# Performance work log

Hardware: AMD Instinct MI355X
Metric: run time of the kernel (lower is better)

## Reference

```python
import jax, jax.numpy as jnp
import numpy as np

DIM = 512
H = 8
HD = DIM // H
SCALE = HD ** (-0.5)


def setup_inputs() -> dict:
    key = jax.random.key(0)
    ks = jax.random.split(key, 10)
    B, Lq, Lp, V = 8, 64, 512, 32
    query = jax.random.normal(ks[0], (B, Lq, DIM), dtype=jnp.float32)
    memory = jax.random.normal(ks[1], (B, Lp, V, DIM), dtype=jnp.float32)
    init = lambda k: jax.random.normal(k, (DIM, DIM), dtype=jnp.float32) * (DIM ** -0.5)
    return {
        "query": query,
        "memory": memory,
        "Wq_c": init(ks[2]),
        "Wk_c": init(ks[3]),
        "Wv_c": init(ks[4]),
        "Wq": init(ks[5]),
        "Wk": init(ks[6]),
        "Wv": init(ks[7]),
        "Wp": init(ks[8]),
        "bp": jnp.zeros((DIM,), dtype=jnp.float32),
    }


def reference(query, memory, Wq_c, Wk_c, Wv_c, Wq, Wk, Wv, Wp, bp):
    B, Lq, d = query.shape
    _, Lp, V, _ = memory.shape
    # ---- stage 1: channel cross-attention over V ----
    qc = (query @ Wq_c).reshape(B, H, Lq, HD)                 # raw view split (faithful)
    kc = (memory @ Wk_c).mean(axis=1).reshape(B, H, V, HD)    # mean over L_p, then view
    vc = (memory @ Wv_c).reshape(B, H, Lp, V, HD)             # 5D value tensor
    # NOTE: original divides by scale = head_dim**-0.5 (i.e. multiplies by sqrt(hd))
    ch_scores = jnp.einsum('bhqd,bhvd->bhqv', qc, kc) / SCALE
    ch_weights = jax.nn.softmax(ch_scores, axis=-1)
    # einsum contracts BOTH q and v (faithful to 'bnqv,bnlvd->bnld')
    ch_out = jnp.einsum('bhqv,bhlvd->bhld', ch_weights, vc)   # (B,H,Lp,HD)
    mem_agg = ch_out.transpose(0, 2, 1, 3).reshape(B, Lp, d)
    # ---- stage 2: standard MHA, query attends to aggregated memory ----
    Q = (query @ Wq).reshape(B, Lq, H, HD).transpose(0, 2, 1, 3)
    K = (mem_agg @ Wk).reshape(B, Lp, H, HD).transpose(0, 2, 1, 3)
    Vv = (mem_agg @ Wv).reshape(B, Lp, H, HD).transpose(0, 2, 1, 3)
    scores = jnp.einsum('bhqd,bhkd->bhqk', Q, K) / SCALE
    weights = jax.nn.softmax(scores, axis=-1)
    attn = jnp.einsum('bhqk,bhkd->bhqd', weights, Vv)
    out = attn.transpose(0, 2, 1, 3).reshape(B, Lq, d)
    return out @ Wp + bp
```

## Files before the change

kernel.cpp:

```cpp
#include <hip/hip_runtime.h>
#include <math.h>

#define NB 8
#define LQ 64
#define LP 512
#define NV 32
#define DIM 512
#define NH 8
#define HD 64

typedef __attribute__((ext_vector_type(4))) float f32x4;
typedef __attribute__((ext_vector_type(8))) short s16x8;

__device__ __forceinline__ unsigned short f2bf(float x) {
  unsigned int u = __float_as_uint(x);
  u += 0x7fff + ((u >> 16) & 1);
  return (unsigned short)(u >> 16);
}
__device__ __forceinline__ float bf2f(unsigned short h) {
  return __uint_as_float(((unsigned int)h) << 16);
}

__global__ __launch_bounds__(256) void k_part(const float* __restrict__ mem,
                                              float* __restrict__ part) {
  int blk = blockIdx.x;
  int bv = blk >> 3, ch = blk & 7;
  int b = bv >> 5, v = bv & 31;
  int tid = threadIdx.x;
  float a0 = 0.f, a1 = 0.f;
  int l0 = ch * 64;
  for (int l = l0; l < l0 + 64; ++l) {
    const float* row = mem + (((size_t)b * LP + l) * NV + v) * DIM;
    a0 += row[tid];
    a1 += row[tid + 256];
  }
  float* dst = part + ((size_t)bv * 8 + ch) * DIM;
  dst[tid] = a0;
  dst[tid + 256] = a1;
}

__global__ __launch_bounds__(256) void k_mean_split(
    const float* __restrict__ part, unsigned short* __restrict__ mh,
    unsigned short* __restrict__ ml) {
  int o = blockIdx.x * 256 + threadIdx.x;
  int bv = o >> 9, c = o & 511;
  float s = 0.f;
#pragma unroll
  for (int ch = 0; ch < 8; ++ch) s += part[((size_t)bv * 8 + ch) * 512 + c];
  s *= (1.0f / 512.0f);
  unsigned short hh = f2bf(s);
  mh[o] = hh;
  ml[o] = f2bf(s - bf2f(hh));
}

__global__ __launch_bounds__(256) void k_splitA(const float* __restrict__ src,
                                                unsigned short* __restrict__ dh,
                                                unsigned short* __restrict__ dl) {
  size_t t = (size_t)blockIdx.x * 256 + threadIdx.x;
  const float* p = src + t * 8;
  s16x8 vh, vl;
#pragma unroll
  for (int q = 0; q < 8; q += 4) {
    float4 x = *(const float4*)(p + q);
    unsigned short h0 = f2bf(x.x), h1 = f2bf(x.y), h2 = f2bf(x.z), h3 = f2bf(x.w);
    vh[q] = (short)h0; vh[q + 1] = (short)h1; vh[q + 2] = (short)h2; vh[q + 3] = (short)h3;
    vl[q] = (short)f2bf(x.x - bf2f(h0));
    vl[q + 1] = (short)f2bf(x.y - bf2f(h1));
    vl[q + 2] = (short)f2bf(x.z - bf2f(h2));
    vl[q + 3] = (short)f2bf(x.w - bf2f(h3));
  }
  *(s16x8*)(dh + t * 8) = vh;
  *(s16x8*)(dl + t * 8) = vl;
}

__global__ __launch_bounds__(256) void k_splitWT(
    const float* W0, const float* W1, const float* W2, const float* W3,
    const float* W4, const float* W5, unsigned short* __restrict__ dh,
    unsigned short* __restrict__ dl) {
  __shared__ float tf[64][65];
  int z = blockIdx.z;
  const float* W = z == 0 ? W0 : z == 1 ? W1 : z == 2 ? W2 : z == 3 ? W3
                 : z == 4 ? W4 : W5;
  unsigned short* oh = dh + (size_t)z * 262144;
  unsigned short* ol = dl + (size_t)z * 262144;
  int r0 = blockIdx.x * 64, c0 = blockIdx.y * 64;
  int tid = threadIdx.x;
  int r = tid >> 2, cs = (tid & 3) * 16;
#pragma unroll
  for (int q = 0; q < 16; q += 4) {
    float4 w4 = *(const float4*)(W + (size_t)(r0 + r) * 512 + c0 + cs + q);
    tf[r][cs + q] = w4.x; tf[r][cs + q + 1] = w4.y;
    tf[r][cs + q + 2] = w4.z; tf[r][cs + q + 3] = w4.w;
  }
  __syncthreads();
  int c = tid >> 2, rs = (tid & 3) * 16;
  s16x8 vh0, vh1, vl0, vl1;
#pragma unroll
  for (int j = 0; j < 16; ++j) {
    float x = tf[rs + j][c];
    unsigned short hh = f2bf(x);
    unsigned short ll = f2bf(x - bf2f(hh));
    if (j < 8) { vh0[j] = (short)hh; vl0[j] = (short)ll; }
    else       { vh1[j - 8] = (short)hh; vl1[j - 8] = (short)ll; }
  }
  size_t off = (size_t)(c0 + c) * 512 + r0 + rs;
  *(s16x8*)(oh + off) = vh0; *(s16x8*)(oh + off + 8) = vh1;
  *(s16x8*)(ol + off) = vl0; *(s16x8*)(ol + off + 8) = vl1;
}

#define STAGE16(dst, src)                                                     \
  do {                                                                        \
    *(s16x8*)((char*)(dst) + sr * 128 + ((sb) ^ swz)) = *(const s16x8*)(src); \
    *(s16x8*)((char*)(dst) + sr * 128 + (((sb) + 16) ^ swz)) =                \
        *(const s16x8*)((src) + 8);                                           \
  } while (0)

#define MFMA_INNER()                                                          \
  do {                                                                        \
    _Pragma("unroll") for (int ks = 0; ks < 2; ++ks) {                        \
      int kb = ks * 64 + kg * 16;                                             \
      s16x8 aH[2], aL[2], bH[2], bL[2];                                       \
      _Pragma("unroll") for (int mt = 0; mt < 2; ++mt) {                      \
        int row = wm + mt * 16 + lr;                                          \
        int off = row * 128 + (kb ^ ((row & 7) << 4));                        \
        aH[mt] = *(const s16x8*)((const char*)AsH + off);                     \
        aL[mt] = *(const s16x8*)((const char*)AsL + off);                     \
      }                                                                       \
      _Pragma("unroll") for (int nt = 0; nt < 2; ++nt) {                      \
        int row = wn + nt * 16 + lr;                                          \
        int off = row * 128 + (kb ^ ((row & 7) << 4));                        \
        bH[nt] = *(const s16x8*)((const char*)BsH + off);                     \
        bL[nt] = *(const s16x8*)((const char*)BsL + off);                     \
      }                                                                       \
      _Pragma("unroll") for (int mt = 0; mt < 2; ++mt)                        \
          _Pragma("unroll") for (int nt = 0; nt < 2; ++nt) {                  \
        acc[mt][nt] = __builtin_amdgcn_mfma_f32_16x16x32_bf16(                \
            aH[mt], bH[nt], acc[mt][nt], 0, 0, 0);                            \
        acc[mt][nt] = __builtin_amdgcn_mfma_f32_16x16x32_bf16(                \
            aH[mt], bL[nt], acc[mt][nt], 0, 0, 0);                            \
        acc[mt][nt] = __builtin_amdgcn_mfma_f32_16x16x32_bf16(                \
            aL[mt], bH[nt], acc[mt][nt], 0, 0, 0);                            \
      }                                                                       \
    }                                                                         \
  } while (0)

__global__ __launch_bounds__(256) void mgemm(
    const unsigned short* __restrict__ Ahi, const unsigned short* __restrict__ Alo,
    const unsigned short* __restrict__ Bhi, const unsigned short* __restrict__ Blo,
    const float* __restrict__ bias, float* __restrict__ C, int K, int ldc) {
  __shared__ unsigned short AsH[64 * 64], AsL[64 * 64], BsH[64 * 64], BsL[64 * 64];
  int tid = threadIdx.x;
  int m0 = blockIdx.x * 64, n0 = blockIdx.y * 64;
  int lane = tid & 63, wave = tid >> 6;
  int wm = (wave >> 1) * 32, wn = (wave & 1) * 32;
  int lr = lane & 15, kg = lane >> 4;
  int sr = tid >> 2, sb = (tid & 3) * 32;
  int swz = (sr & 7) << 4;
  f32x4 acc[2][2] = {};
  const unsigned short* pAh = Ahi + (size_t)(m0 + sr) * K + (sb >> 1);
  const unsigned short* pAl = Alo + (size_t)(m0 + sr) * K + (sb >> 1);
  const unsigned short* pBh = Bhi + (size_t)(n0 + sr) * K + (sb >> 1);
  const unsigned short* pBl = Blo + (size_t)(n0 + sr) * K + (sb >> 1);
  for (int k0 = 0; k0 < K; k0 += 64) {
    STAGE16(AsH, pAh + k0);
    STAGE16(AsL, pAl + k0);
    STAGE16(BsH, pBh + k0);
    STAGE16(BsL, pBl + k0);
    __syncthreads();
    MFMA_INNER();
    __syncthreads();
  }
#pragma unroll
  for (int mt = 0; mt < 2; ++mt)
#pragma unroll
    for (int nt = 0; nt < 2; ++nt) {
      int col = n0 + wn + nt * 16 + lr;
      float badd = bias ? bias[col] : 0.f;
      int rowb = m0 + wm + mt * 16 + kg * 4;
#pragma unroll
      for (int r = 0; r < 4; ++r)
        C[(size_t)(rowb + r) * ldc + col] = acc[mt][nt][r] + badd;
    }
}

__global__ __launch_bounds__(256) void k_ch(const float* __restrict__ qlin,
                                            const float* __restrict__ kclin,
                                            float* __restrict__ wsum) {
  __shared__ float qcs[4096];
  __shared__ float kcs[2048];
  __shared__ float sc[2048];
  int bh = blockIdx.x;
  int b = bh >> 3, h = bh & 7;
  int tid = threadIdx.x;
  const float* qsrc = qlin + ((size_t)b * LQ + h * 8) * DIM;
  for (int s = tid; s < 4096; s += 256) qcs[s] = qsrc[s];
  const float* ksrc = kclin + ((size_t)b * NV + h * 4) * DIM;
  for (int s = tid; s < 2048; s += 256) kcs[s] = ksrc[s];
  __syncthreads();
  for (int s = tid; s < 2048; s += 256) {
    int q = s >> 5, v = s & 31;
    float acc = 0.f;
#pragma unroll 8
    for (int d = 0; d < 64; ++d) acc = fmaf(qcs[q * 64 + d], kcs[v * 64 + d], acc);
    sc[s] = acc * 8.0f;
  }
  __syncthreads();
  if (tid < 64) {
    int q = tid;
    float m = -INFINITY;
    for (int v = 0; v < 32; ++v) m = fmaxf(m, sc[q * 32 + v]);
    float sum = 0.f;
    for (int v = 0; v < 32; ++v) {
      float e = __expf(sc[q * 32 + v] - m);
      sc[q * 32 + v] = e;
      sum += e;
    }
    float inv = 1.0f / sum;
    for (int v = 0; v < 32; ++v) sc[q * 32 + v] *= inv;
  }
  __syncthreads();
  if (tid < 32) {
    float s = 0.f;
    for (int q = 0; q < 64; ++q) s += sc[q * 32 + tid];
    wsum[(size_t)bh * 32 + tid] = s;
  }
}

__global__ __launch_bounds__(256) void k_weff(const float* __restrict__ wsum,
                                              const float* __restrict__ Wv_c,
                                              unsigned short* __restrict__ wth,
                                              unsigned short* __restrict__ wtl) {
  __shared__ float tf[64][65];
  int bh = blockIdx.x >> 2, a = blockIdx.x & 3;
  int tid = threadIdx.x;
  float wsv[8];
#pragma unroll
  for (int r = 0; r < 8; ++r) wsv[r] = wsum[(size_t)bh * 32 + a * 8 + r];
  int cl = tid >> 2, hg = (tid & 3) * 16;
  int hd = tid >> 2, cs = (tid & 3) * 16;
  for (int c0 = 0; c0 < 512; c0 += 64) {
    float v[16] = {};
#pragma unroll
    for (int r = 0; r < 8; ++r) {
      const float* wp = Wv_c + (size_t)(c0 + cl) * 512 + r * 64 + hg;
#pragma unroll
      for (int j = 0; j < 16; j += 4) {
        float4 w4 = *(const float4*)(wp + j);
        v[j] = fmaf(wsv[r], w4.x, v[j]);
        v[j + 1] = fmaf(wsv[r], w4.y, v[j + 1]);
        v[j + 2] = fmaf(wsv[r], w4.z, v[j + 2]);
        v[j + 3] = fmaf(wsv[r], w4.w, v[j + 3]);
      }
    }
    __syncthreads();
#pragma unroll
    for (int j = 0; j < 16; ++j) tf[cl][hg + j] = v[j];
    __syncthreads();
    s16x8 vh0, vh1, vl0, vl1;
#pragma unroll
    for (int j = 0; j < 16; ++j) {
      float x = tf[cs + j][hd];
      unsigned short hh = f2bf(x);
      unsigned short ll = f2bf(x - bf2f(hh));
      if (j < 8) { vh0[j] = (short)hh; vl0[j] = (short)ll; }
      else       { vh1[j - 8] = (short)hh; vl1[j - 8] = (short)ll; }
    }
    size_t off = ((size_t)bh * 64 + hd) * 2048 + a * 512 + c0 + cs;
    *(s16x8*)(wth + off) = vh0; *(s16x8*)(wth + off + 8) = vh1;
    *(s16x8*)(wtl + off) = vl0; *(s16x8*)(wtl + off + 8) = vl1;
  }
}

__global__ __launch_bounds__(256) void k_stage1m(
    const float* __restrict__ mem, const unsigned short* __restrict__ WTh,
    const unsigned short* __restrict__ WTl, unsigned short* __restrict__ mgh,
    unsigned short* __restrict__ mgl) {
  __shared__ unsigned short AsH[64 * 64], AsL[64 * 64], BsH[64 * 64], BsL[64 * 64];
  int P = blockIdx.x;
  int blk = (P & 7) * 64 + (P >> 3);
  int b = blk >> 6, h = (blk >> 3) & 7, i = blk & 7;
  int bh = b * 8 + h;
  int tid = threadIdx.x;
  int lane = tid & 63, wave = tid >> 6;
  int wm = (wave >> 1) * 32, wn = (wave & 1) * 32;
  int lr = lane & 15, kg = lane >> 4;
  int sr = tid >> 2, sb = (tid & 3) * 32;
  int swz = (sr & 7) << 4;
  f32x4 acc[2][2] = {};
  const float* abase =
      mem + ((size_t)(b * 512 + h * 64 + sr) * 32 + 4 * i) * 512 + (tid & 3) * 16;
  const unsigned short* bbh = WTh + ((size_t)bh * 64 + sr) * 2048 + (sb >> 1);
  const unsigned short* bbl = WTl + ((size_t)bh * 64 + sr) * 2048 + (sb >> 1);
  for (int k0 = 0; k0 < 2048; k0 += 64) {
    s16x8 vh0, vh1, vl0, vl1;
#pragma unroll
    for (int q = 0; q < 16; q += 4) {
      float4 x = *(const float4*)(abase + k0 + q);
      unsigned short h0 = f2bf(x.x), h1 = f2bf(x.y), h2 = f2bf(x.z), h3 = f2bf(x.w);
      unsigned short l0 = f2bf(x.x - bf2f(h0)), l1 = f2bf(x.y - bf2f(h1));
      unsigned short l2 = f2bf(x.z - bf2f(h2)), l3 = f2bf(x.w - bf2f(h3));
      if (q < 8) {
        vh0[q] = (short)h0; vh0[q + 1] = (short)h1; vh0[q + 2] = (short)h2; vh0[q + 3] = (short)h3;
        vl0[q] = (short)l0; vl0[q + 1] = (short)l1; vl0[q + 2] = (short)l2; vl0[q + 3] = (short)l3;
      } else {
        vh1[q - 8] = (short)h0; vh1[q - 7] = (short)h1; vh1[q - 6] = (short)h2; vh1[q - 5] = (short)h3;
        vl1[q - 8] = (short)l0; vl1[q - 7] = (short)l1; vl1[q - 6] = (short)l2; vl1[q - 5] = (short)l3;
      }
    }
    *(s16x8*)((char*)AsH + sr * 128 + (sb ^ swz)) = vh0;
    *(s16x8*)((char*)AsH + sr * 128 + ((sb + 16) ^ swz)) = vh1;
    *(s16x8*)((char*)AsL + sr * 128 + (sb ^ swz)) = vl0;
    *(s16x8*)((char*)AsL + sr * 128 + ((sb + 16) ^ swz)) = vl1;
    STAGE16(BsH, bbh + k0);
    STAGE16(BsL, bbl + k0);
    __syncthreads();
    MFMA_INNER();
    __syncthreads();
  }
#pragma unroll
  for (int mt = 0; mt < 2; ++mt)
#pragma unroll
    for (int nt = 0; nt < 2; ++nt) {
      int hd = wn + nt * 16 + lr;
      int jb = wm + mt * 16 + kg * 4;
#pragma unroll
      for (int r = 0; r < 4; ++r) {
        int j = jb + r;
        size_t idx = ((size_t)b * 512 + 8 * j + i) * 512 + h * 64 + hd;
        float v = acc[mt][nt][r];
        unsigned short hh = f2bf(v);
        mgh[idx] = hh;
        mgl[idx] = f2bf(v - bf2f(hh));
      }
    }
}

__global__ __launch_bounds__(256) void k_attn(const float* __restrict__ q2,
                                              const float* __restrict__ kmat,
                                              const float* __restrict__ vmat,
                                              unsigned short* __restrict__ ath,
                                              unsigned short* __restrict__ atl) {
  __shared__ float Qs[4096];
  __shared__ float Ks[4096];
  __shared__ float Vs[4096];
  int bh = blockIdx.x;
  int b = bh >> 3, h = bh & 7;
  int tid = threadIdx.x;
  for (int s = tid; s < 4096; s += 256) {
    int q = s >> 6, hd = s & 63;
    Qs[s] = q2[((size_t)b * LQ + q) * DIM + h * 64 + hd];
  }
  __syncthreads();
  int qr = tid >> 2, quad = tid & 3;
  float qreg[16];
#pragma unroll
  for (int j = 0; j < 16; ++j) qreg[j] = Qs[qr * 64 + quad * 16 + j];
  float m = -INFINITY, l = 0.f;
  float acc[16] = {};
  for (int kt = 0; kt < 8; ++kt) {
    __syncthreads();
    for (int s = tid; s < 4096; s += 256) {
      int kk = s >> 6, hd = s & 63;
      size_t src = ((size_t)b * LP + kt * 64 + kk) * DIM + h * 64 + hd;
      Ks[s] = kmat[src];
      Vs[s] = vmat[src];
    }
    __syncthreads();
    for (int kk = 0; kk < 64; ++kk) {
      float p = 0.f;
      const float* kr = &Ks[kk * 64 + quad * 16];
#pragma unroll
      for (int j = 0; j < 16; ++j) p = fmaf(qreg[j], kr[j], p);
      p += __shfl_xor(p, 1);
      p += __shfl_xor(p, 2);
      float sco = p * 8.0f;
      float nm = fmaxf(m, sco);
      float co = __expf(m - nm);
      float po = __expf(sco - nm);
      l = l * co + po;
      const float* vr = &Vs[kk * 64 + quad * 16];
#pragma unroll
      for (int j = 0; j < 16; ++j) acc[j] = fmaf(po, vr[j], acc[j] * co);
      m = nm;
    }
  }
  float inv = 1.0f / l;
  s16x8 vh0, vh1, vl0, vl1;
#pragma unroll
  for (int j = 0; j < 16; ++j) {
    float o = acc[j] * inv;
    unsigned short hh = f2bf(o);
    unsigned short ll = f2bf(o - bf2f(hh));
    if (j < 8) { vh0[j] = (short)hh; vl0[j] = (short)ll; }
    else       { vh1[j - 8] = (short)hh; vl1[j - 8] = (short)ll; }
  }
  size_t ob = ((size_t)b * LQ + qr) * DIM + h * 64 + quad * 16;
  *(s16x8*)(ath + ob) = vh0; *(s16x8*)(ath + ob + 8) = vh1;
  *(s16x8*)(atl + ob) = vl0; *(s16x8*)(atl + ob + 8) = vl1;
}

extern "C" void kernel_launch(void* const* d_in, const int* in_sizes, int n_in,
                              void* d_out, int out_size, void* d_ws,
                              size_t ws_size, hipStream_t stream) {
  const float* query = (const float*)d_in[0];
  const float* memory = (const float*)d_in[1];
  const float* Wq_c = (const float*)d_in[2];
  const float* Wk_c = (const float*)d_in[3];
  const float* Wv_c = (const float*)d_in[4];
  const float* Wq = (const float*)d_in[5];
  const float* Wk = (const float*)d_in[6];
  const float* Wv = (const float*)d_in[7];
  const float* Wp = (const float*)d_in[8];
  const float* bp = (const float*)d_in[9];
  float* out = (float*)d_out;
  float* ws = (float*)d_ws;

  float* part = ws;
  float* qlin = ws;
  float* kclin = ws + 262144;
  float* q2 = ws + 393216;
  unsigned short* ath = (unsigned short*)(ws + 655360);
  unsigned short* atl = (unsigned short*)(ws + 786432);
  unsigned short* mmh = (unsigned short*)(ws + 1048576);
  unsigned short* mml = (unsigned short*)(ws + 1114112);
  unsigned short* qh = (unsigned short*)(ws + 1179648);
  unsigned short* ql = (unsigned short*)(ws + 1310720);
  unsigned short* WTh = (unsigned short*)(ws + 1441792);
  unsigned short* WTl = (unsigned short*)(ws + 2228224);
  float* wsum = ws + 3014656;
  unsigned short* wth = (unsigned short*)(ws + 3016704);
  unsigned short* wtl = (unsigned short*)(ws + 7211008);
  float* kmat = ws + 3016704;
  float* vmat = ws + 5113856;
  unsigned short* mgh = (unsigned short*)(ws + 11405312);
  unsigned short* mgl = (unsigned short*)(ws + 12453888);

  k_part<<<2048, 256, 0, stream>>>(memory, part);
  k_mean_split<<<512, 256, 0, stream>>>(part, mmh, mml);

  k_splitA<<<128, 256, 0, stream>>>(query, qh, ql);
  k_splitWT<<<dim3(8, 8, 6), 256, 0, stream>>>(Wq_c, Wk_c, Wq, Wk, Wv, Wp,
                                               WTh, WTl);

  mgemm<<<dim3(8, 8), 256, 0, stream>>>(qh, ql, WTh, WTl, nullptr, qlin, 512, 512);
  mgemm<<<dim3(4, 8), 256, 0, stream>>>(mmh, mml, WTh + 262144, WTl + 262144,
                                        nullptr, kclin, 512, 512);

  k_ch<<<64, 256, 0, stream>>>(qlin, kclin, wsum);
  k_weff<<<256, 256, 0, stream>>>(wsum, Wv_c, wth, wtl);

  k_stage1m<<<512, 256, 0, stream>>>(memory, wth, wtl, mgh, mgl);

  mgemm<<<dim3(8, 8), 256, 0, stream>>>(qh, ql, WTh + 2 * 262144,
                                        WTl + 2 * 262144, nullptr, q2, 512, 512);
  mgemm<<<dim3(64, 8), 256, 0, stream>>>(mgh, mgl, WTh + 3 * 262144,
                                         WTl + 3 * 262144, nullptr, kmat, 512, 512);
  mgemm<<<dim3(64, 8), 256, 0, stream>>>(mgh, mgl, WTh + 4 * 262144,
                                         WTl + 4 * 262144, nullptr, vmat, 512, 512);

  k_attn<<<64, 256, 0, stream>>>(q2, kmat, vmat, ath, atl);
  mgemm<<<dim3(8, 8), 256, 0, stream>>>(ath, atl, WTh + 5 * 262144,
                                        WTl + 5 * 262144, bp, out, 512, 512);
}
```

Before: 705.5 us.

## Double-buffer GEMM tiles and pre-split memory into bf16 hi/lo during mean pass

The GEMM kernels now use double-buffered shared memory with register prefetch of the next K tile, so global loads overlap the MFMA work on the current tile. The memory-mean pass also writes truncated bf16 hi/lo copies of the whole memory tensor, which lets the stage-1 GEMM load pre-split bf16 data instead of converting fp32 in its inner loop. This adds a large extra write of the memory tensor (about the same size as the fp32 input) and a re-read later, and the hi/lo split now truncates instead of rounding to nearest. Shared memory per block doubles, which may reduce occupancy.

```diff
diff --git a/kernel.cpp b/kernel.cpp
--- a/kernel.cpp
+++ b/kernel.cpp
@@ -21,8 +21,9 @@
   return __uint_as_float(((unsigned int)h) << 16);
 }
 
-__global__ __launch_bounds__(256) void k_part(const float* __restrict__ mem,
-                                              float* __restrict__ part) {
+__global__ __launch_bounds__(256) void k_part_split(
+    const float* __restrict__ mem, float* __restrict__ part,
+    unsigned short* __restrict__ memh, unsigned short* __restrict__ meml) {
   int blk = blockIdx.x;
   int bv = blk >> 3, ch = blk & 7;
   int b = bv >> 5, v = bv & 31;
@@ -30,9 +31,20 @@
   float a0 = 0.f, a1 = 0.f;
   int l0 = ch * 64;
   for (int l = l0; l < l0 + 64; ++l) {
-    const float* row = mem + (((size_t)b * LP + l) * NV + v) * DIM;
-    a0 += row[tid];
-    a1 += row[tid + 256];
+    size_t base = (((size_t)b * LP + l) * NV + v) * DIM;
+    float x0 = mem[base + tid];
+    float x1 = mem[base + tid + 256];
+    a0 += x0;
+    a1 += x1;
+    unsigned int u0 = __float_as_uint(x0), u1 = __float_as_uint(x1);
+    unsigned short h0 = (unsigned short)(u0 >> 16);
+    unsigned short h1 = (unsigned short)(u1 >> 16);
+    float lo0 = x0 - __uint_as_float(u0 & 0xffff0000u);
+    float lo1 = x1 - __uint_as_float(u1 & 0xffff0000u);
+    memh[base + tid] = h0;
+    memh[base + tid + 256] = h1;
+    meml[base + tid] = (unsigned short)(__float_as_uint(lo0) >> 16);
+    meml[base + tid + 256] = (unsigned short)(__float_as_uint(lo1) >> 16);
   }
   float* dst = part + ((size_t)bv * 8 + ch) * DIM;
   dst[tid] = a0;
@@ -108,14 +120,31 @@
   *(s16x8*)(ol + off) = vl0; *(s16x8*)(ol + off + 8) = vl1;
 }
 
-#define STAGE16(dst, src)                                                     \
-  do {                                                                        \
-    *(s16x8*)((char*)(dst) + sr * 128 + ((sb) ^ swz)) = *(const s16x8*)(src); \
-    *(s16x8*)((char*)(dst) + sr * 128 + (((sb) + 16) ^ swz)) =                \
-        *(const s16x8*)((src) + 8);                                           \
+#define GLOAD(k0)                                \
+  do {                                           \
+    pf[0] = *(const s16x8*)(pAh + (k0));         \
+    pf[1] = *(const s16x8*)(pAh + (k0) + 8);     \
+    pf[2] = *(const s16x8*)(pAl + (k0));         \
+    pf[3] = *(const s16x8*)(pAl + (k0) + 8);     \
+    pf[4] = *(const s16x8*)(pBh + (k0));         \
+    pf[5] = *(const s16x8*)(pBh + (k0) + 8);     \
+    pf[6] = *(const s16x8*)(pBl + (k0));         \
+    pf[7] = *(const s16x8*)(pBl + (k0) + 8);     \
   } while (0)
 
-#define MFMA_INNER()                                                          \
+#define SWRITE(buf)                                                        \
+  do {                                                                     \
+    *(s16x8*)((char*)AsH[buf] + sr * 128 + (sb ^ swz)) = pf[0];            \
+    *(s16x8*)((char*)AsH[buf] + sr * 128 + ((sb + 16) ^ swz)) = pf[1];     \
+    *(s16x8*)((char*)AsL[buf] + sr * 128 + (sb ^ swz)) = pf[2];            \
+    *(s16x8*)((char*)AsL[buf] + sr * 128 + ((sb + 16) ^ swz)) = pf[3];     \
+    *(s16x8*)((char*)BsH[buf] + sr * 128 + (sb ^ swz)) = pf[4];            \
+    *(s16x8*)((char*)BsH[buf] + sr * 128 + ((sb + 16) ^ swz)) = pf[5];     \
+    *(s16x8*)((char*)BsL[buf] + sr * 128 + (sb ^ swz)) = pf[6];            \
+    *(s16x8*)((char*)BsL[buf] + sr * 128 + ((sb + 16) ^ swz)) = pf[7];     \
+  } while (0)
+
+#define MFMA_INNER(buf)                                                       \
   do {                                                                        \
     _Pragma("unroll") for (int ks = 0; ks < 2; ++ks) {                        \
       int kb = ks * 64 + kg * 16;                                             \
@@ -123,14 +152,14 @@
       _Pragma("unroll") for (int mt = 0; mt < 2; ++mt) {                      \
         int row = wm + mt * 16 + lr;                                          \
         int off = row * 128 + (kb ^ ((row & 7) << 4));                        \
-        aH[mt] = *(const s16x8*)((const char*)AsH + off);                     \
-        aL[mt] = *(const s16x8*)((const char*)AsL + off);                     \
+        aH[mt] = *(const s16x8*)((const char*)AsH[buf] + off);                \
+        aL[mt] = *(const s16x8*)((const char*)AsL[buf] + off);                \
       }                                                                       \
       _Pragma("unroll") for (int nt = 0; nt < 2; ++nt) {                      \
         int row = wn + nt * 16 + lr;                                          \
         int off = row * 128 + (kb ^ ((row & 7) << 4));                        \
-        bH[nt] = *(const s16x8*)((const char*)BsH + off);                     \
-        bL[nt] = *(const s16x8*)((const char*)BsL + off);                     \
+        bH[nt] = *(const s16x8*)((const char*)BsH[buf] + off);                \
+        bL[nt] = *(const s16x8*)((const char*)BsL[buf] + off);                \
       }                                                                       \
       _Pragma("unroll") for (int mt = 0; mt < 2; ++mt)                        \
           _Pragma("unroll") for (int nt = 0; nt < 2; ++nt) {                  \
@@ -144,30 +173,36 @@
     }                                                                         \
   } while (0)
 
+#define GEMM_PREAMBLE()                       \
+  int tid = threadIdx.x;                      \
+  int lane = tid & 63, wave = tid >> 6;       \
+  int wm = (wave >> 1) * 32, wn = (wave & 1) * 32; \
+  int lr = lane & 15, kg = lane >> 4;         \
+  int sr = tid >> 2, sb = (tid & 3) * 32;     \
+  int swz = (sr & 7) << 4;                    \
+  f32x4 acc[2][2] = {};                       \
+  s16x8 pf[8];
+
 __global__ __launch_bounds__(256) void mgemm(
     const unsigned short* __restrict__ Ahi, const unsigned short* __restrict__ Alo,
     const unsigned short* __restrict__ Bhi, const unsigned short* __restrict__ Blo,
     const float* __restrict__ bias, float* __restrict__ C, int K, int ldc) {
-  __shared__ unsigned short AsH[64 * 64], AsL[64 * 64], BsH[64 * 64], BsL[64 * 64];
-  int tid = threadIdx.x;
+  __shared__ unsigned short AsH[2][4096], AsL[2][4096], BsH[2][4096], BsL[2][4096];
+  GEMM_PREAMBLE();
   int m0 = blockIdx.x * 64, n0 = blockIdx.y * 64;
-  int lane = tid & 63, wave = tid >> 6;
-  int wm = (wave >> 1) * 32, wn = (wave & 1) * 32;
-  int lr = lane & 15, kg = lane >> 4;
-  int sr = tid >> 2, sb = (tid & 3) * 32;
-  int swz = (sr & 7) << 4;
-  f32x4 acc[2][2] = {};
   const unsigned short* pAh = Ahi + (size_t)(m0 + sr) * K + (sb >> 1);
   const unsigned short* pAl = Alo + (size_t)(m0 + sr) * K + (sb >> 1);
   const unsigned short* pBh = Bhi + (size_t)(n0 + sr) * K + (sb >> 1);
   const unsigned short* pBl = Blo + (size_t)(n0 + sr) * K + (sb >> 1);
-  for (int k0 = 0; k0 < K; k0 += 64) {
-    STAGE16(AsH, pAh + k0);
-    STAGE16(AsL, pAl + k0);
-    STAGE16(BsH, pBh + k0);
-    STAGE16(BsL, pBl + k0);
-    __syncthreads();
-    MFMA_INNER();
+  int NT = K >> 6;
+  GLOAD(0);
+  SWRITE(0);
+  __syncthreads();
+  for (int t = 0; t < NT; ++t) {
+    int cur = t & 1;
+    if (t + 1 < NT) GLOAD((t + 1) * 64);
+    MFMA_INNER(cur);
+    if (t + 1 < NT) SWRITE(cur ^ 1);
     __syncthreads();
   }
 #pragma unroll
@@ -272,49 +307,29 @@
 }
 
 __global__ __launch_bounds__(256) void k_stage1m(
-    const float* __restrict__ mem, const unsigned short* __restrict__ WTh,
-    const unsigned short* __restrict__ WTl, unsigned short* __restrict__ mgh,
-    unsigned short* __restrict__ mgl) {
-  __shared__ unsigned short AsH[64 * 64], AsL[64 * 64], BsH[64 * 64], BsL[64 * 64];
+    const unsigned short* __restrict__ Amh, const unsigned short* __restrict__ Aml,
+    const unsigned short* __restrict__ WTh, const unsigned short* __restrict__ WTl,
+    unsigned short* __restrict__ mgh, unsigned short* __restrict__ mgl) {
+  __shared__ unsigned short AsH[2][4096], AsL[2][4096], BsH[2][4096], BsL[2][4096];
+  GEMM_PREAMBLE();
   int P = blockIdx.x;
   int blk = (P & 7) * 64 + (P >> 3);
   int b = blk >> 6, h = (blk >> 3) & 7, i = blk & 7;
   int bh = b * 8 + h;
-  int tid = threadIdx.x;
-  int lane = tid & 63, wave = tid >> 6;
-  int wm = (wave >> 1) * 32, wn = (wave & 1) * 32;
-  int lr = lane & 15, kg = lane >> 4;
-  int sr = tid >> 2, sb = (tid & 3) * 32;
-  int swz = (sr & 7) << 4;
-  f32x4 acc[2][2] = {};
-  const float* abase =
-      mem + ((size_t)(b * 512 + h * 64 + sr) * 32 + 4 * i) * 512 + (tid & 3) * 16;
-  const unsigned short* bbh = WTh + ((size_t)bh * 64 + sr) * 2048 + (sb >> 1);
-  const unsigned short* bbl = WTl + ((size_t)bh * 64 + sr) * 2048 + (sb >> 1);
-  for (int k0 = 0; k0 < 2048; k0 += 64) {
-    s16x8 vh0, vh1, vl0, vl1;
-#pragma unroll
-    for (int q = 0; q < 16; q += 4) {
-      float4 x = *(const float4*)(abase + k0 + q);
-      unsigned short h0 = f2bf(x.x), h1 = f2bf(x.y), h2 = f2bf(x.z), h3 = f2bf(x.w);
-      unsigned short l0 = f2bf(x.x - bf2f(h0)), l1 = f2bf(x.y - bf2f(h1));
-      unsigned short l2 = f2bf(x.z - bf2f(h2)), l3 = f2bf(x.w - bf2f(h3));
-      if (q < 8) {
-        vh0[q] = (short)h0; vh0[q + 1] = (short)h1; vh0[q + 2] = (short)h2; vh0[q + 3] = (short)h3;
-        vl0[q] = (short)l0; vl0[q + 1] = (short)l1; vl0[q + 2] = (short)l2; vl0[q + 3] = (short)l3;
-      } else {
-        vh1[q - 8] = (short)h0; vh1[q - 7] = (short)h1; vh1[q - 6] = (short)h2; vh1[q - 5] = (short)h3;
-        vl1[q - 8] = (short)l0; vl1[q - 7] = (short)l1; vl1[q - 6] = (short)l2; vl1[q - 5] = (short)l3;
-      }
-    }
-    *(s16x8*)((char*)AsH + sr * 128 + (sb ^ swz)) = vh0;
-    *(s16x8*)((char*)AsH + sr * 128 + ((sb + 16) ^ swz)) = vh1;
-    *(s16x8*)((char*)AsL + sr * 128 + (sb ^ swz)) = vl0;
-    *(s16x8*)((char*)AsL + sr * 128 + ((sb + 16) ^ swz)) = vl1;
-    STAGE16(BsH, bbh + k0);
-    STAGE16(BsL, bbl + k0);
-    __syncthreads();
-    MFMA_INNER();
+  size_t arow = ((size_t)(b * 512 + h * 64 + sr) * 32 + 4 * i) * 512 + (sb >> 1);
+  const unsigned short* pAh = Amh + arow;
+  const unsigned short* pAl = Aml + arow;
+  const unsigned short* pBh = WTh + ((size_t)bh * 64 + sr) * 2048 + (sb >> 1);
+  const unsigned short* pBl = WTl + ((size_t)bh * 64 + sr) * 2048 + (sb >> 1);
+  const int NT = 32;
+  GLOAD(0);
+  SWRITE(0);
+  __syncthreads();
+  for (int t = 0; t < NT; ++t) {
+    int cur = t & 1;
+    if (t + 1 < NT) GLOAD((t + 1) * 64);
+    MFMA_INNER(cur);
+    if (t + 1 < NT) SWRITE(cur ^ 1);
     __syncthreads();
   }
 #pragma unroll
@@ -434,8 +449,10 @@
   float* vmat = ws + 5113856;
   unsigned short* mgh = (unsigned short*)(ws + 11405312);
   unsigned short* mgl = (unsigned short*)(ws + 12453888);
-
-  k_part<<<2048, 256, 0, stream>>>(memory, part);
+  unsigned short* memh = (unsigned short*)(ws + 13502464);
+  unsigned short* meml = (unsigned short*)(ws + 47056896);
+
+  k_part_split<<<2048, 256, 0, stream>>>(memory, part, memh, meml);
   k_mean_split<<<512, 256, 0, stream>>>(part, mmh, mml);
 
   k_splitA<<<128, 256, 0, stream>>>(query, qh, ql);
@@ -449,7 +466,7 @@
   k_ch<<<64, 256, 0, stream>>>(qlin, kclin, wsum);
   k_weff<<<256, 256, 0, stream>>>(wsum, Wv_c, wth, wtl);
 
-  k_stage1m<<<512, 256, 0, stream>>>(memory, wth, wtl, mgh, mgl);
+  k_stage1m<<<512, 256, 0, stream>>>(memh, meml, wth, wtl, mgh, mgl);
 
   mgemm<<<dim3(8, 8), 256, 0, stream>>>(qh, ql, WTh + 2 * 262144,
                                         WTl + 2 * 262144, nullptr, q2, 512, 512);
```

New measurement: 738.0 us. +4.6%, slower.
